# Kernel tuning notes

Measured on AMD Instinct MI355X. Metric: run time of the kernel, lower is better.

Reference implementation:

```python
import jax, jax.numpy as jnp
import numpy as np

MAX_DISP = 128
STRIDE2 = 1


def setup_inputs() -> dict:
    key = jax.random.key(0)
    k1, k2 = jax.random.split(key)
    B, C, H, W = 4, 32, 256, 512
    in1 = jax.random.normal(k1, (B, C, H, W), dtype=jnp.float32)
    in2 = jax.random.normal(k2, (B, C, H, W), dtype=jnp.float32)
    return {"in1": in1, "in2": in2}


def reference(in1, in2):
    # Pad in2 on the left of the width axis by MAX_DISP zeros
    # (torch ConstantPad2d((max_disp, 0, 0, 0), 0)).
    D = MAX_DISP
    W = in1.shape[3]
    in2_pad = jnp.pad(in2, ((0, 0), (0, 0), (0, 0), (D, 0)))

    offsets = jnp.arange(0, D, STRIDE2)

    def corr_at(dx):
        # slice in2_pad[:, :, :, dx:dx+W] and channel-mean the product
        sl = jax.lax.dynamic_slice_in_dim(in2_pad, dx, W, axis=3)
        return jnp.mean(in1 * sl, axis=1)  # [B, H, W]

    # vmap over disparity offsets -> output [B, D, H, W]
    out = jax.vmap(corr_at, out_axes=1)(offsets)
    return out
```

## Files before the change

### kernel.cpp

```cpp
#include <hip/hip_runtime.h>


#define BB 4
#define CC 32
#define HH 256
#define WW 512
#define DD 128
#define HW (HH * WW)

#define NT 512
#define WHALF 256
#define S2N 384
#define OBW 136

typedef __attribute__((ext_vector_type(8))) short bf16x8;
typedef __attribute__((ext_vector_type(4))) float f32x4;
typedef __attribute__((ext_vector_type(2))) float f32x2;

__device__ __forceinline__ unsigned int pk2(float lo, float hi) {
    union { float f; unsigned int i; } x, y; x.f = lo; y.f = hi;
    unsigned int xi = x.i + 0x7fffu + ((x.i >> 16) & 1u);
    unsigned int yi = y.i + 0x7fffu + ((y.i >> 16) & 1u);
    return (xi >> 16) | (yi & 0xffff0000u);
}
__device__ __forceinline__ unsigned short pk1(float v) {
    union { float f; unsigned int i; } x; x.f = v;
    return (unsigned short)((x.i + 0x7fffu + ((x.i >> 16) & 1u)) >> 16);
}

__device__ __forceinline__ int cidx(int row, int kc) {
    return (row * 4 + (kc ^ ((row >> 1) & 3))) * 4;
}

__global__ __launch_bounds__(NT, 2)
void disp_corr_kernel(const float* __restrict__ in1,
                      const float* __restrict__ in2,
                      float* __restrict__ out) {
    __shared__ __align__(16) unsigned int s1t[WHALF * 16];
    __shared__ __align__(16) unsigned int s2t[S2N * 16];
    __shared__ __align__(16) unsigned short obs[DD * OBW];

    const int t = threadIdx.x;

    const int xcd = blockIdx.x & 7, slot = blockIdx.x >> 3;
    const int work = (xcd << 8) + slot;
    const int wh = work & 1;
    const int h  = (work >> 1) & (HH - 1);
    const int b  = work >> 9;
    const int wb = wh * WHALF;

    const float* p1 = in1 + (size_t)b * CC * HW + (size_t)h * WW + wb;
    const float* p2 = in2 + (size_t)b * CC * HW + (size_t)h * WW;
    const float sc = 1.0f / (float)CC;

    {
        const bool one = (t < 256);
        const int u  = one ? t : t - 256;
        const int kc = u >> 6;
        const int wg = u & 63;
        float l[8][4];
        if (one) {
            #pragma unroll
            for (int ci = 0; ci < 8; ++ci)
                *(float4*)l[ci] =
                    *(const float4*)(p1 + (size_t)(kc * 8 + ci) * HW + wg * 4);
            #pragma unroll
            for (int ci = 0; ci < 8; ++ci)
                #pragma unroll
                for (int rr = 0; rr < 4; ++rr) l[ci][rr] *= sc;
        } else {
            const int wp = wb + wg * 4 - DD;
            if (wp >= 0) {
                #pragma unroll
                for (int ci = 0; ci < 8; ++ci)
                    *(float4*)l[ci] =
                        *(const float4*)(p2 + (size_t)(kc * 8 + ci) * HW + wp);
            } else {
                #pragma unroll
                for (int ci = 0; ci < 8; ++ci)
                    #pragma unroll
                    for (int rr = 0; rr < 4; ++rr) l[ci][rr] = 0.f;
            }
        }
        #pragma unroll
        for (int rr = 0; rr < 4; ++rr) {
            const int row = wg * 4 + rr;
            const uint4 uu = make_uint4(pk2(l[0][rr], l[1][rr]),
                                        pk2(l[2][rr], l[3][rr]),
                                        pk2(l[4][rr], l[5][rr]),
                                        pk2(l[6][rr], l[7][rr]));
            unsigned int* dst = one ? &s1t[cidx(row, kc)] : &s2t[cidx(row, kc)];
            *(uint4*)dst = uu;
        }
    }
    if (t < 128) {
        const int kc = t >> 5;
        const int wg = 64 + (t & 31);
        const int wp = wb + wg * 4 - DD;
        float l[8][4];
        #pragma unroll
        for (int ci = 0; ci < 8; ++ci)
            *(float4*)l[ci] =
                *(const float4*)(p2 + (size_t)(kc * 8 + ci) * HW + wp);
        #pragma unroll
        for (int rr = 0; rr < 4; ++rr) {
            const int row = wg * 4 + rr;
            const uint4 uu = make_uint4(pk2(l[0][rr], l[1][rr]),
                                        pk2(l[2][rr], l[3][rr]),
                                        pk2(l[4][rr], l[5][rr]),
                                        pk2(l[6][rr], l[7][rr]));
            *(uint4*)&s2t[cidx(row, kc)] = uu;
        }
    }
    __syncthreads();

    const int lane = t & 63;
    const int wv   = t >> 6;
    const int cl   = lane & 15;
    const int rg   = lane >> 4;
    const size_t obase = (size_t)b * DD * HW + (size_t)h * WW + wb;

    #pragma unroll
    for (int ro = 0; ro < 2; ++ro) {
        const int i = ro * 8 + wv;
        union { uint4 u; bf16x8 v; } a;
        a.u = *(const uint4*)&s1t[cidx(i * 16 + cl, rg)];
        #pragma unroll
        for (int mm = 0; mm <= 8; ++mm) {
            union { uint4 u; bf16x8 v; } bq;
            bq.u = *(const uint4*)&s2t[cidx((i + mm) * 16 + cl, rg)];
            f32x4 acc = {0.f, 0.f, 0.f, 0.f};
            acc = __builtin_amdgcn_mfma_f32_16x16x32_bf16(a.v, bq.v, acc, 0, 0, 0);
            #pragma unroll
            for (int q = 0; q < 4; ++q) {
                const int r = rg * 4 + q;
                const int d = mm * 16 + cl - r;
                const bool ok = (mm == 0) ? (cl >= r)
                              : (mm == 8) ? (cl < r) : true;
                if (ok) obs[d * OBW + wv * 16 + r] = pk1(acc[q]);
            }
        }
        __syncthreads();
        const float* op0 = out + obase + 128 * ro;
        #pragma unroll
        for (int p = 0; p < 16; ++p) {
            const int d = wv * 16 + p;
            const unsigned int u = *(const unsigned int*)&obs[d * OBW + 2 * lane];
            union { unsigned int i; float f; } lo, hi;
            lo.i = u << 16;
            hi.i = u & 0xffff0000u;
            f32x2 v = {lo.f, hi.f};
            __builtin_nontemporal_store(
                v, (f32x2*)(op0 + (size_t)d * HW + 2 * lane));
        }
        __syncthreads();
    }
}

extern "C" void kernel_launch(void* const* d_in, const int* in_sizes, int n_in,
                              void* d_out, int out_size, void* d_ws, size_t ws_size,
                              hipStream_t stream) {
    const float* in1 = (const float*)d_in[0];
    const float* in2 = (const float*)d_in[1];
    float* out = (float*)d_out;
    const int nblocks = BB * HH * 2;
    disp_corr_kernel<<<nblocks, NT, 0, stream>>>(in1, in2, out);
}
```

Measured before the change: 66.55 us.

## Process full image row per block and load in1 fragments directly into registers

Each block now handles a whole width row instead of half, so the overlapping in2 halo (128 columns) is loaded once per row rather than twice, cutting redundant in2 traffic. The in1 A-fragments are read straight from global memory into registers in MFMA layout, removing the s1t shared buffer and its LDS round trip. The trade-off is half as many blocks (1024), larger per-block LDS for in2, scalar strided in1 loads, and more registers per thread, which may hurt occupancy and latency hiding.

```diff
diff --git a/kernel.cpp b/kernel.cpp
--- a/kernel.cpp
+++ b/kernel.cpp
@@ -9,8 +9,7 @@
 #define HW (HH * WW)
 
 #define NT 512
-#define WHALF 256
-#define S2N 384
+#define S2N 640
 #define OBW 136
 
 typedef __attribute__((ext_vector_type(8))) short bf16x8;
@@ -36,40 +35,47 @@
 void disp_corr_kernel(const float* __restrict__ in1,
                       const float* __restrict__ in2,
                       float* __restrict__ out) {
-    __shared__ __align__(16) unsigned int s1t[WHALF * 16];
     __shared__ __align__(16) unsigned int s2t[S2N * 16];
     __shared__ __align__(16) unsigned short obs[DD * OBW];
 
     const int t = threadIdx.x;
 
     const int xcd = blockIdx.x & 7, slot = blockIdx.x >> 3;
-    const int work = (xcd << 8) + slot;
-    const int wh = work & 1;
-    const int h  = (work >> 1) & (HH - 1);
-    const int b  = work >> 9;
-    const int wb = wh * WHALF;
+    const int work = (xcd << 7) + slot;
+    const int h  = work & (HH - 1);
+    const int b  = work >> 8;
 
-    const float* p1 = in1 + (size_t)b * CC * HW + (size_t)h * WW + wb;
+    const float* p1 = in1 + (size_t)b * CC * HW + (size_t)h * WW;
     const float* p2 = in2 + (size_t)b * CC * HW + (size_t)h * WW;
     const float sc = 1.0f / (float)CC;
 
+    const int lane = t & 63;
+    const int wv   = t >> 6;
+    const int cl   = lane & 15;
+    const int rg   = lane >> 4;
+
+    uint4 afr[4];
     {
-        const bool one = (t < 256);
-        const int u  = one ? t : t - 256;
-        const int kc = u >> 6;
-        const int wg = u & 63;
-        float l[8][4];
-        if (one) {
+        const int w0 = wv * 16 + cl;
+        #pragma unroll
+        for (int ro = 0; ro < 4; ++ro) {
+            float f[8];
             #pragma unroll
             for (int ci = 0; ci < 8; ++ci)
-                *(float4*)l[ci] =
-                    *(const float4*)(p1 + (size_t)(kc * 8 + ci) * HW + wg * 4);
-            #pragma unroll
-            for (int ci = 0; ci < 8; ++ci)
-                #pragma unroll
-                for (int rr = 0; rr < 4; ++rr) l[ci][rr] *= sc;
-        } else {
-            const int wp = wb + wg * 4 - DD;
+                f[ci] = p1[(size_t)(rg * 8 + ci) * HW + ro * 128 + w0] * sc;
+            afr[ro] = make_uint4(pk2(f[0], f[1]), pk2(f[2], f[3]),
+                                 pk2(f[4], f[5]), pk2(f[6], f[7]));
+        }
+    }
+
+    #pragma unroll
+    for (int k = 0; k < 2; ++k) {
+        const int u = t + k * NT;
+        if (u < 640) {
+            const int kc = u & 3;
+            const int wg = u >> 2;
+            const int wp = wg * 4 - DD;
+            float l[8][4];
             if (wp >= 0) {
                 #pragma unroll
                 for (int ci = 0; ci < 8; ++ci)
@@ -81,50 +87,26 @@
                     #pragma unroll
                     for (int rr = 0; rr < 4; ++rr) l[ci][rr] = 0.f;
             }
-        }
-        #pragma unroll
-        for (int rr = 0; rr < 4; ++rr) {
-            const int row = wg * 4 + rr;
-            const uint4 uu = make_uint4(pk2(l[0][rr], l[1][rr]),
-                                        pk2(l[2][rr], l[3][rr]),
-                                        pk2(l[4][rr], l[5][rr]),
-                                        pk2(l[6][rr], l[7][rr]));
-            unsigned int* dst = one ? &s1t[cidx(row, kc)] : &s2t[cidx(row, kc)];
-            *(uint4*)dst = uu;
-        }
-    }
-    if (t < 128) {
-        const int kc = t >> 5;
-        const int wg = 64 + (t & 31);
-        const int wp = wb + wg * 4 - DD;
-        float l[8][4];
-        #pragma unroll
-        for (int ci = 0; ci < 8; ++ci)
-            *(float4*)l[ci] =
-                *(const float4*)(p2 + (size_t)(kc * 8 + ci) * HW + wp);
-        #pragma unroll
-        for (int rr = 0; rr < 4; ++rr) {
-            const int row = wg * 4 + rr;
-            const uint4 uu = make_uint4(pk2(l[0][rr], l[1][rr]),
-                                        pk2(l[2][rr], l[3][rr]),
-                                        pk2(l[4][rr], l[5][rr]),
-                                        pk2(l[6][rr], l[7][rr]));
-            *(uint4*)&s2t[cidx(row, kc)] = uu;
+            #pragma unroll
+            for (int rr = 0; rr < 4; ++rr) {
+                const int row = wg * 4 + rr;
+                const uint4 uu = make_uint4(pk2(l[0][rr], l[1][rr]),
+                                            pk2(l[2][rr], l[3][rr]),
+                                            pk2(l[4][rr], l[5][rr]),
+                                            pk2(l[6][rr], l[7][rr]));
+                *(uint4*)&s2t[cidx(row, kc)] = uu;
+            }
         }
     }
     __syncthreads();
 
-    const int lane = t & 63;
-    const int wv   = t >> 6;
-    const int cl   = lane & 15;
-    const int rg   = lane >> 4;
-    const size_t obase = (size_t)b * DD * HW + (size_t)h * WW + wb;
+    const size_t obase = (size_t)b * DD * HW + (size_t)h * WW;
 
     #pragma unroll
-    for (int ro = 0; ro < 2; ++ro) {
+    for (int ro = 0; ro < 4; ++ro) {
         const int i = ro * 8 + wv;
         union { uint4 u; bf16x8 v; } a;
-        a.u = *(const uint4*)&s1t[cidx(i * 16 + cl, rg)];
+        a.u = afr[ro];
         #pragma unroll
         for (int mm = 0; mm <= 8; ++mm) {
             union { uint4 u; bf16x8 v; } bq;
@@ -163,6 +145,6 @@
     const float* in1 = (const float*)d_in[0];
     const float* in2 = (const float*)d_in[1];
     float* out = (float*)d_out;
-    const int nblocks = BB * HH * 2;
+    const int nblocks = BB * HH;
     disp_corr_kernel<<<nblocks, NT, 0, stream>>>(in1, in2, out);
 }
```

Result: no change. 67.47 us (+1.4%).
